# Optimization experiments

Hardware: AMD Instinct MI355X
Metric: run time of the kernel (lower is better)

Reference implementation:

```python
import jax, jax.numpy as jnp
import numpy as np


def conv1x1(x, w, b):
    # x: [B, Cin, H, W], w: [Cout, Cin], b: [Cout]
    return jnp.einsum('oc,bchw->bohw', w, x) + b[None, :, None, None]


def setup_inputs() -> dict:
    key = jax.random.key(0)
    ks = jax.random.split(key, 10)
    B, C, H, W = 8, 256, 64, 64
    C2 = C // 2
    s = 1.0 / np.sqrt(C)
    s2 = 1.0 / np.sqrt(C2)
    return {
        'x1': jax.random.normal(ks[0], (B, C, H, W), jnp.float32),
        'x2': jax.random.normal(ks[1], (B, C, H, W), jnp.float32),
        'w_th': jax.random.uniform(ks[2], (C2, C), jnp.float32, -s, s),
        'b_th': jax.random.uniform(ks[3], (C2,), jnp.float32, -s, s),
        'w_pi': jax.random.uniform(ks[4], (C2, C), jnp.float32, -s, s),
        'b_pi': jax.random.uniform(ks[5], (C2,), jnp.float32, -s, s),
        'w_g': jax.random.uniform(ks[6], (C2, C), jnp.float32, -s, s),
        'b_g': jax.random.uniform(ks[7], (C2,), jnp.float32, -s, s),
        'w_out': jax.random.uniform(ks[8], (C, C2), jnp.float32, -s2, s2),
        'b_out': jax.random.uniform(ks[9], (C,), jnp.float32, -s2, s2),
    }


def reference(x1, x2, w_th, b_th, w_pi, b_pi, w_g, b_g, w_out, b_out):
    B, C, H, W = x1.shape
    HW = H * W
    res = x1
    # 1x1 conv projections -> [B, C2, HW]
    e1 = conv1x1(x1, w_th, b_th).reshape(B, -1, HW)  # theta
    e2 = conv1x1(x2, w_pi, b_pi).reshape(B, -1, HW)  # phi
    # scores: [B, HW, HW]
    f = jnp.einsum('bcq,bck->bqk', e1, e2)
    # GLOBAL softmax over the whole HWxHW matrix per batch element
    f = jax.nn.softmax(f.reshape(B, HW * HW), axis=1).reshape(B, HW, HW)
    g2 = conv1x1(x2, w_g, b_g).reshape(B, -1, HW)  # [B, C2, HW]
    # out = f @ g2^T -> [B, HW, C2] -> [B, C2, H, W]
    out = jnp.einsum('bqk,bck->bcq', f, g2).reshape(B, -1, H, W)
    out = conv1x1(out, w_out, b_out)
    return out + res
```

## Files before the change

kernel.cpp:

```cpp
#include <hip/hip_runtime.h>

typedef unsigned short u16;
typedef short s16x8 __attribute__((ext_vector_type(8)));
typedef float f32x4 __attribute__((ext_vector_type(4)));

#define HWN 4096
#define CC  256
#define C2  128

static __device__ __forceinline__ u16 f2bf(float f) {
    union { float f; unsigned int u; } c; c.f = f;
    unsigned int u = c.u;
    unsigned int r = (u + 0x7fffu + ((u >> 16) & 1u)) >> 16;
    return (u16)r;
}
static __device__ __forceinline__ float bf2f(u16 u) {
    union { unsigned int u; float f; } c; c.u = ((unsigned int)u) << 16; return c.f;
}

__global__ __launch_bounds__(256) void k_wcvt(
    const float* __restrict__ w_th, const float* __restrict__ w_pi,
    const float* __restrict__ w_g,  const float* __restrict__ w_out,
    u16* __restrict__ wthb, u16* __restrict__ wpib,
    u16* __restrict__ wgb,  u16* __restrict__ woutb)
{
    int i = blockIdx.x * 256 + threadIdx.x;
    wthb[i]  = f2bf(w_th[i]);
    wpib[i]  = f2bf(w_pi[i]);
    wgb[i]   = f2bf(w_g[i]);
    woutb[i] = f2bf(w_out[i]);
}

__device__ __forceinline__ void load_afrag(const float* __restrict__ px, int g, s16x8 a[8]) {
    #pragma unroll
    for (int ks = 0; ks < 8; ++ks) {
        union { s16x8 v; u16 u[8]; } c;
        #pragma unroll
        for (int j = 0; j < 8; ++j)
            c.u[j] = f2bf(px[(size_t)(ks*32 + g*8 + j) * HWN]);
        a[ks] = c.v;
    }
}

__device__ __forceinline__ void proj_gemm(const s16x8 a[8], const u16* __restrict__ wb,
                                          const float* __restrict__ bias,
                                          int m16, int g, f32x4 acc[8]) {
    #pragma unroll
    for (int nb = 0; nb < 8; ++nb) {
        float bv = bias[nb*16 + m16];
        acc[nb] = (f32x4){bv, bv, bv, bv};
    }
    #pragma unroll
    for (int ks = 0; ks < 8; ++ks) {
        #pragma unroll
        for (int nb = 0; nb < 8; ++nb) {
            s16x8 bb = *(const s16x8*)&wb[(size_t)(nb*16 + m16)*CC + ks*32 + g*8];
            acc[nb] = __builtin_amdgcn_mfma_f32_16x16x32_bf16(a[ks], bb, acc[nb], 0, 0, 0);
        }
    }
}

__global__ __launch_bounds__(256) void k_projM(
    const float* __restrict__ x1, const float* __restrict__ x2,
    const u16* __restrict__ wthb, const float* __restrict__ b_th,
    const u16* __restrict__ wpib, const float* __restrict__ b_pi,
    const u16* __restrict__ wgb,  const float* __restrict__ b_g,
    u16* __restrict__ e1t, u16* __restrict__ e2t, u16* __restrict__ g2c)
{
    __shared__ u16 gs[C2][72];
    const int tid  = threadIdx.x;
    const int b    = blockIdx.x >> 6;
    const int q0   = (blockIdx.x & 63) * 64;
    const int wid  = __builtin_amdgcn_readfirstlane(tid >> 6);
    const int lane = tid & 63;
    const int m16  = lane & 15;
    const int g    = lane >> 4;

    s16x8 a[8];
    f32x4 acc[8];

    const float* px1 = x1 + (size_t)b*CC*HWN + q0 + wid*16 + m16;
    load_afrag(px1, g, a);
    proj_gemm(a, wthb, b_th, m16, g, acc);
    #pragma unroll
    for (int nb = 0; nb < 8; ++nb)
        #pragma unroll
        for (int r = 0; r < 4; ++r)
            e1t[((size_t)b*HWN + q0 + wid*16 + g*4 + r)*C2 + nb*16 + m16] = f2bf(acc[nb][r]);

    const float* px2 = x2 + (size_t)b*CC*HWN + q0 + wid*16 + m16;
    load_afrag(px2, g, a);
    proj_gemm(a, wpib, b_pi, m16, g, acc);
    #pragma unroll
    for (int nb = 0; nb < 8; ++nb)
        #pragma unroll
        for (int r = 0; r < 4; ++r)
            e2t[((size_t)b*HWN + q0 + wid*16 + g*4 + r)*C2 + nb*16 + m16] = f2bf(acc[nb][r]);

    proj_gemm(a, wgb, b_g, m16, g, acc);
    #pragma unroll
    for (int nb = 0; nb < 8; ++nb)
        #pragma unroll
        for (int r = 0; r < 4; ++r)
            gs[nb*16 + m16][wid*16 + g*4 + r] = f2bf(acc[nb][r]);
    __syncthreads();
    #pragma unroll
    for (int r = 0; r < 4; ++r) {
        int idx = r*256 + tid;
        int c2 = idx >> 3, q8 = idx & 7;
        int4 v = *(const int4*)&gs[c2][q8*8];
        *(int4*)&g2c[((size_t)b*C2 + c2)*HWN + q0 + q8*8] = v;
    }
}

__global__ __launch_bounds__(256, 2) void k_flash(
    const u16* __restrict__ e1t, const u16* __restrict__ e2t,
    const u16* __restrict__ g2c,
    u16* __restrict__ outp0, u16* __restrict__ outp1, float* __restrict__ ms)
{
    __shared__ u16 e2s[64*128];
    __shared__ u16 g2s[128*64];
    __shared__ u16 ps[4][32*64];

    const int tid  = threadIdx.x;
    const int b    = blockIdx.x >> 6;
    const int qb   = (blockIdx.x >> 1) & 31;
    const int seg  = blockIdx.x & 1;
    const int q0   = qb * 128;
    const int wid  = __builtin_amdgcn_readfirstlane(tid >> 6);
    const int lane = tid & 63;
    const int m16  = lane & 15;
    const int g    = lane >> 4;
    const int sw16 = (m16 & 7) << 3;

    s16x8 af[2][4];
    #pragma unroll
    for (int h = 0; h < 2; ++h) {
        const u16* p = e1t + ((size_t)b*HWN + q0 + wid*32 + h*16 + m16)*C2 + g*8;
        #pragma unroll
        for (int kc = 0; kc < 4; ++kc) af[h][kc] = *(const s16x8*)(p + kc*32);
    }

    f32x4 acc[2][8];
    #pragma unroll
    for (int h = 0; h < 2; ++h)
        #pragma unroll
        for (int i = 0; i < 8; ++i) acc[h][i] = (f32x4){0.f,0.f,0.f,0.f};
    float m_w = -INFINITY, s_w = 0.f;

    const u16* e2base = e2t + (size_t)b*HWN*C2;
    const u16* g2base = g2c + (size_t)b*C2*HWN;
    const int er_row = tid >> 4, er_c16 = tid & 15;
    const int gr_row = tid >> 3, gr_c8  = tid & 7;

    for (int it = 0; it < 32; ++it) {
        const int k0 = seg*2048 + it*64;
        __syncthreads();
        #pragma unroll
        for (int r = 0; r < 4; ++r) {
            int row = r*16 + er_row;
            int4 v = *(const int4*)(e2base + (size_t)(k0 + row)*C2 + er_c16*8);
            *(int4*)&e2s[(row*128 + er_c16*8) ^ ((row&7)<<3)] = v;
        }
        #pragma unroll
        for (int r = 0; r < 4; ++r) {
            int row = r*32 + gr_row;
            int4 v = *(const int4*)(g2base + (size_t)row*HWN + k0 + gr_c8*8);
            *(int4*)&g2s[(row*64 + gr_c8*8) ^ ((row&7)<<3)] = v;
        }
        __syncthreads();

        f32x4 s[2][4];
        #pragma unroll
        for (int h = 0; h < 2; ++h)
            #pragma unroll
            for (int j = 0; j < 4; ++j) s[h][j] = (f32x4){0.f,0.f,0.f,0.f};
        #pragma unroll
        for (int j = 0; j < 4; ++j) {
            #pragma unroll
            for (int kc = 0; kc < 4; ++kc) {
                s16x8 bb = *(const s16x8*)&e2s[((j*16+m16)*128 + kc*32 + g*8) ^ sw16];
                s[0][j] = __builtin_amdgcn_mfma_f32_16x16x32_bf16(af[0][kc], bb, s[0][j], 0, 0, 0);
                s[1][j] = __builtin_amdgcn_mfma_f32_16x16x32_bf16(af[1][kc], bb, s[1][j], 0, 0, 0);
            }
        }
        float tm = -INFINITY;
        #pragma unroll
        for (int h = 0; h < 2; ++h)
            #pragma unroll
            for (int j = 0; j < 4; ++j)
                #pragma unroll
                for (int r = 0; r < 4; ++r) tm = fmaxf(tm, s[h][j][r]);
        #pragma unroll
        for (int off = 32; off >= 1; off >>= 1) tm = fmaxf(tm, __shfl_xor(tm, off));
        const float m_new = fmaxf(m_w, tm);
        const float scale = __expf(m_w - m_new);
        m_w = m_new;
        s_w *= scale;
        #pragma unroll
        for (int h = 0; h < 2; ++h)
            #pragma unroll
            for (int i = 0; i < 8; ++i) {
                acc[h][i][0] *= scale; acc[h][i][1] *= scale;
                acc[h][i][2] *= scale; acc[h][i][3] *= scale;
            }
        float psum = 0.f;
        #pragma unroll
        for (int h = 0; h < 2; ++h)
            #pragma unroll
            for (int j = 0; j < 4; ++j)
                #pragma unroll
                for (int r = 0; r < 4; ++r) {
                    float p = __expf(s[h][j][r] - m_new);
                    psum += p;
                    int qq = h*16 + g*4 + r;
                    ps[wid][(qq*64 + j*16 + m16) ^ ((qq&7)<<3)] = f2bf(p);
                }
        s_w += psum;
        #pragma unroll
        for (int kk = 0; kk < 2; ++kk) {
            s16x8 pa0 = *(const s16x8*)&ps[wid][(m16*64      + kk*32 + g*8) ^ sw16];
            s16x8 pa1 = *(const s16x8*)&ps[wid][((16+m16)*64 + kk*32 + g*8) ^ sw16];
            #pragma unroll
            for (int fc = 0; fc < 8; ++fc) {
                s16x8 gb = *(const s16x8*)&g2s[((fc*16+m16)*64 + kk*32 + g*8) ^ sw16];
                acc[0][fc] = __builtin_amdgcn_mfma_f32_16x16x32_bf16(pa0, gb, acc[0][fc], 0, 0, 0);
                acc[1][fc] = __builtin_amdgcn_mfma_f32_16x16x32_bf16(pa1, gb, acc[1][fc], 0, 0, 0);
            }
        }
    }

    #pragma unroll
    for (int off = 32; off >= 1; off >>= 1) s_w += __shfl_xor(s_w, off);
    if (lane == 0) {
        int idx = b*256 + seg*128 + qb*4 + wid;
        ms[idx*2 + 0] = m_w;
        ms[idx*2 + 1] = s_w;
    }
    const float inv_s = 1.f / s_w;
    u16* op = seg ? outp1 : outp0;
    #pragma unroll
    for (int h = 0; h < 2; ++h)
        #pragma unroll
        for (int fc = 0; fc < 8; ++fc)
            #pragma unroll
            for (int r = 0; r < 4; ++r)
                op[((size_t)b*HWN + q0 + wid*32 + h*16 + g*4 + r)*C2 + fc*16 + m16] =
                    f2bf(acc[h][fc][r] * inv_s);
}

__global__ void k_mz(const float* __restrict__ ms, float* __restrict__ mz)
{
    __shared__ float rmax[4], rsum[4];
    const int b = blockIdx.x, tid = threadIdx.x;
    const int lane = tid & 63, wid = tid >> 6;
    float m = ms[((size_t)b*256 + tid)*2 + 0];
    float s = ms[((size_t)b*256 + tid)*2 + 1];
    float mm = m;
    #pragma unroll
    for (int off = 32; off >= 1; off >>= 1) mm = fmaxf(mm, __shfl_xor(mm, off));
    if (lane == 0) rmax[wid] = mm;
    __syncthreads();
    float M = fmaxf(fmaxf(rmax[0], rmax[1]), fmaxf(rmax[2], rmax[3]));
    float z = s * __expf(m - M);
    #pragma unroll
    for (int off = 32; off >= 1; off >>= 1) z += __shfl_xor(z, off);
    if (lane == 0) rsum[wid] = z;
    __syncthreads();
    if (tid == 0) { mz[b*2] = M; mz[b*2+1] = rsum[0]+rsum[1]+rsum[2]+rsum[3]; }
}

__global__ __launch_bounds__(256) void k_outM(
    const u16* __restrict__ outp0, const u16* __restrict__ outp1,
    const float* __restrict__ ms, const float* __restrict__ mz,
    const u16* __restrict__ woutb, const float* __restrict__ b_out,
    const float* __restrict__ x1, float* __restrict__ out)
{
    const int tid  = threadIdx.x;
    const int b    = blockIdx.x >> 6;
    const int q0   = (blockIdx.x & 63) * 64;
    const int wv   = tid >> 6;
    const int lane = tid & 63;
    const int m16  = lane & 15;
    const int g    = lane >> 4;
    const int q    = q0 + wv*16 + m16;

    const float M    = mz[b*2];
    const float invZ = 1.f / mz[b*2+1];
    const int idx5   = (q0 >> 5) + (wv >> 1);
    const float a0 = ms[(b*256 + idx5)*2+1]       * __expf(ms[(b*256 + idx5)*2]       - M) * invZ;
    const float a1 = ms[(b*256 + 128 + idx5)*2+1] * __expf(ms[(b*256 + 128 + idx5)*2] - M) * invZ;

    s16x8 bfr[4];
    #pragma unroll
    for (int ks = 0; ks < 4; ++ks) {
        union { s16x8 v; u16 u[8]; } o0, o1, oc;
        o0.v = *(const s16x8*)&outp0[((size_t)b*HWN + q)*C2 + ks*32 + g*8];
        o1.v = *(const s16x8*)&outp1[((size_t)b*HWN + q)*C2 + ks*32 + g*8];
        #pragma unroll
        for (int j = 0; j < 8; ++j)
            oc.u[j] = f2bf(a0*bf2f(o0.u[j]) + a1*bf2f(o1.u[j]));
        bfr[ks] = oc.v;
    }

    f32x4 acc[16];
    #pragma unroll
    for (int cb = 0; cb < 16; ++cb) acc[cb] = (f32x4){0.f,0.f,0.f,0.f};
    #pragma unroll
    for (int ks = 0; ks < 4; ++ks) {
        #pragma unroll
        for (int cb = 0; cb < 16; ++cb) {
            s16x8 afr = *(const s16x8*)&woutb[(size_t)(cb*16 + m16)*C2 + ks*32 + g*8];
            acc[cb] = __builtin_amdgcn_mfma_f32_16x16x32_bf16(afr, bfr[ks], acc[cb], 0, 0, 0);
        }
    }

    #pragma unroll
    for (int cb = 0; cb < 16; ++cb) {
        f32x4 bb = *(const f32x4*)&b_out[cb*16 + g*4];
        #pragma unroll
        for (int r = 0; r < 4; ++r) {
            int co = cb*16 + g*4 + r;
            size_t o = ((size_t)b*CC + co)*HWN + q;
            out[o] = acc[cb][r] + bb[r] + x1[o];
        }
    }
}

extern "C" void kernel_launch(void* const* d_in, const int* in_sizes, int n_in,
                              void* d_out, int out_size, void* d_ws, size_t ws_size,
                              hipStream_t stream)
{
    const float* x1   = (const float*)d_in[0];
    const float* x2   = (const float*)d_in[1];
    const float* w_th = (const float*)d_in[2];
    const float* b_th = (const float*)d_in[3];
    const float* w_pi = (const float*)d_in[4];
    const float* b_pi = (const float*)d_in[5];
    const float* w_g  = (const float*)d_in[6];
    const float* b_g  = (const float*)d_in[7];
    const float* w_out= (const float*)d_in[8];
    const float* b_out= (const float*)d_in[9];
    float* out = (float*)d_out;

    char* ws = (char*)d_ws;
    u16*   e1t  = (u16*)(ws);
    u16*   e2t  = (u16*)(ws + 8388608);
    u16*   g2c  = (u16*)(ws + 16777216);
    u16*   outp0= (u16*)(ws + 25165824);
    u16*   outp1= (u16*)(ws + 33554432);
    float* ms   = (float*)(ws + 41943040);
    float* mz   = (float*)(ws + 41959424);
    u16*   wthb = (u16*)(ws + 41959488);
    u16*   wpib = (u16*)(ws + 42025024);
    u16*   wgb  = (u16*)(ws + 42090560);
    u16*   woutb= (u16*)(ws + 42156096);

    k_wcvt <<<dim3(128), dim3(256), 0, stream>>>(w_th, w_pi, w_g, w_out, wthb, wpib, wgb, woutb);
    k_projM<<<dim3(512), dim3(256), 0, stream>>>(x1, x2, wthb, b_th, wpib, b_pi, wgb, b_g,
                                                 e1t, e2t, g2c);
    k_flash<<<dim3(512), dim3(256), 0, stream>>>(e1t, e2t, g2c, outp0, outp1, ms);
    k_mz   <<<dim3(8),   dim3(256), 0, stream>>>(ms, mz);
    k_outM <<<dim3(512), dim3(256), 0, stream>>>(outp0, outp1, ms, mz, woutb, b_out, x1, out);
}
```

Before: 207.7 us.

## Rework flash kernel with 32x32 MFMA, register P, double-buffered LDS

```diff
diff --git a/kernel.cpp b/kernel.cpp
--- a/kernel.cpp
+++ b/kernel.cpp
@@ -1,21 +1,28 @@
 #include <hip/hip_runtime.h>
 
 typedef unsigned short u16;
+typedef unsigned int u32;
 typedef short s16x8 __attribute__((ext_vector_type(8)));
 typedef float f32x4 __attribute__((ext_vector_type(4)));
+typedef float f32x16 __attribute__((ext_vector_type(16)));
 
 #define HWN 4096
 #define CC  256
 #define C2  128
 
 static __device__ __forceinline__ u16 f2bf(float f) {
-    union { float f; unsigned int u; } c; c.f = f;
-    unsigned int u = c.u;
-    unsigned int r = (u + 0x7fffu + ((u >> 16) & 1u)) >> 16;
+    union { float f; u32 u; } c; c.f = f;
+    u32 u = c.u;
+    u32 r = (u + 0x7fffu + ((u >> 16) & 1u)) >> 16;
     return (u16)r;
 }
 static __device__ __forceinline__ float bf2f(u16 u) {
-    union { unsigned int u; float f; } c; c.u = ((unsigned int)u) << 16; return c.f;
+    union { u32 u; float f; } c; c.u = ((u32)u) << 16; return c.f;
+}
+static __device__ __forceinline__ u32 cvtpk(float lo, float hi) {
+    u32 d;
+    asm("v_cvt_pk_bf16_f32 %0, %1, %2" : "=v"(d) : "v"(lo), "v"(hi));
+    return d;
 }
 
 __global__ __launch_bounds__(256) void k_wcvt(
@@ -118,115 +125,142 @@
     const u16* __restrict__ g2c,
     u16* __restrict__ outp0, u16* __restrict__ outp1, float* __restrict__ ms)
 {
-    __shared__ u16 e2s[64*128];
-    __shared__ u16 g2s[128*64];
-    __shared__ u16 ps[4][32*64];
+    __shared__ u16 e2s[2][64*128];
+    __shared__ u16 g2s[2][128*64];
 
     const int tid  = threadIdx.x;
-    const int b    = blockIdx.x >> 6;
-    const int qb   = (blockIdx.x >> 1) & 31;
-    const int seg  = blockIdx.x & 1;
+    const int bid  = ((blockIdx.x & 7) << 6) | (blockIdx.x >> 3);
+    const int b    = bid >> 6;
+    const int qb   = (bid >> 1) & 31;
+    const int seg  = bid & 1;
     const int q0   = qb * 128;
     const int wid  = __builtin_amdgcn_readfirstlane(tid >> 6);
     const int lane = tid & 63;
-    const int m16  = lane & 15;
-    const int g    = lane >> 4;
-    const int sw16 = (m16 & 7) << 3;
-
-    s16x8 af[2][4];
-    #pragma unroll
-    for (int h = 0; h < 2; ++h) {
-        const u16* p = e1t + ((size_t)b*HWN + q0 + wid*32 + h*16 + m16)*C2 + g*8;
-        #pragma unroll
-        for (int kc = 0; kc < 4; ++kc) af[h][kc] = *(const s16x8*)(p + kc*32);
-    }
-
-    f32x4 acc[2][8];
-    #pragma unroll
-    for (int h = 0; h < 2; ++h)
-        #pragma unroll
-        for (int i = 0; i < 8; ++i) acc[h][i] = (f32x4){0.f,0.f,0.f,0.f};
+    const int l31  = lane & 31;
+    const int h    = lane >> 5;
+    const int swz  = (l31 & 7) << 3;
+
+    s16x8 bq[8];
+    {
+        const u16* p = e1t + ((size_t)b*HWN + q0 + wid*32 + l31)*C2 + h*8;
+        #pragma unroll
+        for (int ks = 0; ks < 8; ++ks) bq[ks] = *(const s16x8*)(p + ks*16);
+    }
+
+    f32x16 accT[4];
+    #pragma unroll
+    for (int i = 0; i < 4; ++i)
+        accT[i] = (f32x16){0,0,0,0,0,0,0,0,0,0,0,0,0,0,0,0};
     float m_w = -INFINITY, s_w = 0.f;
 
     const u16* e2base = e2t + (size_t)b*HWN*C2;
     const u16* g2base = g2c + (size_t)b*C2*HWN;
-    const int er_row = tid >> 4, er_c16 = tid & 15;
-    const int gr_row = tid >> 3, gr_c8  = tid & 7;
+    const int er = tid >> 4, ec = tid & 15;
+    const int gr = tid >> 3, gc = tid & 7;
+    int ew[4], gw[4];
+    #pragma unroll
+    for (int r = 0; r < 4; ++r) {
+        int row = r*16 + er; ew[r] = (row*128 + ec*8) ^ ((row & 7) << 3);
+        int rw  = r*32 + gr; gw[r] = (rw*64  + gc*8) ^ ((rw  & 7) << 3);
+    }
+
+    int4 se[4], sg[4];
+    {
+        const int k0 = seg*2048;
+        #pragma unroll
+        for (int r = 0; r < 4; ++r)
+            se[r] = *(const int4*)(e2base + (size_t)(k0 + r*16 + er)*C2 + ec*8);
+        #pragma unroll
+        for (int r = 0; r < 4; ++r)
+            sg[r] = *(const int4*)(g2base + (size_t)(r*32 + gr)*HWN + k0 + gc*8);
+        #pragma unroll
+        for (int r = 0; r < 4; ++r) *(int4*)&e2s[0][ew[r]] = se[r];
+        #pragma unroll
+        for (int r = 0; r < 4; ++r) *(int4*)&g2s[0][gw[r]] = sg[r];
+    }
 
     for (int it = 0; it < 32; ++it) {
-        const int k0 = seg*2048 + it*64;
+        const int cur = it & 1;
         __syncthreads();
-        #pragma unroll
-        for (int r = 0; r < 4; ++r) {
-            int row = r*16 + er_row;
-            int4 v = *(const int4*)(e2base + (size_t)(k0 + row)*C2 + er_c16*8);
-            *(int4*)&e2s[(row*128 + er_c16*8) ^ ((row&7)<<3)] = v;
-        }
-        #pragma unroll
-        for (int r = 0; r < 4; ++r) {
-            int row = r*32 + gr_row;
-            int4 v = *(const int4*)(g2base + (size_t)row*HWN + k0 + gr_c8*8);
-            *(int4*)&g2s[(row*64 + gr_c8*8) ^ ((row&7)<<3)] = v;
-        }
-        __syncthreads();
-
-        f32x4 s[2][4];
-        #pragma unroll
-        for (int h = 0; h < 2; ++h)
-            #pragma unroll
-            for (int j = 0; j < 4; ++j) s[h][j] = (f32x4){0.f,0.f,0.f,0.f};
-        #pragma unroll
-        for (int j = 0; j < 4; ++j) {
-            #pragma unroll
-            for (int kc = 0; kc < 4; ++kc) {
-                s16x8 bb = *(const s16x8*)&e2s[((j*16+m16)*128 + kc*32 + g*8) ^ sw16];
-                s[0][j] = __builtin_amdgcn_mfma_f32_16x16x32_bf16(af[0][kc], bb, s[0][j], 0, 0, 0);
-                s[1][j] = __builtin_amdgcn_mfma_f32_16x16x32_bf16(af[1][kc], bb, s[1][j], 0, 0, 0);
+        const bool more = (it + 1 < 32);
+        if (more) {
+            const int k0n = seg*2048 + (it+1)*64;
+            #pragma unroll
+            for (int r = 0; r < 4; ++r)
+                se[r] = *(const int4*)(e2base + (size_t)(k0n + r*16 + er)*C2 + ec*8);
+            #pragma unroll
+            for (int r = 0; r < 4; ++r)
+                sg[r] = *(const int4*)(g2base + (size_t)(r*32 + gr)*HWN + k0n + gc*8);
+        }
+
+        f32x16 sr[2];
+        sr[0] = (f32x16){0,0,0,0,0,0,0,0,0,0,0,0,0,0,0,0};
+        sr[1] = (f32x16){0,0,0,0,0,0,0,0,0,0,0,0,0,0,0,0};
+        __builtin_amdgcn_s_setprio(1);
+        #pragma unroll
+        for (int ks = 0; ks < 8; ++ks) {
+            #pragma unroll
+            for (int mt = 0; mt < 2; ++mt) {
+                const int row = mt*32 + l31;
+                s16x8 afr = *(const s16x8*)&e2s[cur][row*128 + ((ks*16 + h*8) ^ swz)];
+                sr[mt] = __builtin_amdgcn_mfma_f32_32x32x16_bf16(afr, bq[ks], sr[mt], 0, 0, 0);
             }
         }
+        __builtin_amdgcn_s_setprio(0);
+
         float tm = -INFINITY;
         #pragma unroll
-        for (int h = 0; h < 2; ++h)
-            #pragma unroll
-            for (int j = 0; j < 4; ++j)
+        for (int mt = 0; mt < 2; ++mt)
+            #pragma unroll
+            for (int r = 0; r < 16; ++r) tm = fmaxf(tm, sr[mt][r]);
+        #pragma unroll
+        for (int off = 32; off >= 1; off >>= 1) tm = fmaxf(tm, __shfl_xor(tm, off));
+        if (tm > m_w + 8.f) {
+            const float sc = __expf(m_w - tm);
+            s_w *= sc;
+            #pragma unroll
+            for (int mt = 0; mt < 4; ++mt)
                 #pragma unroll
-                for (int r = 0; r < 4; ++r) tm = fmaxf(tm, s[h][j][r]);
-        #pragma unroll
-        for (int off = 32; off >= 1; off >>= 1) tm = fmaxf(tm, __shfl_xor(tm, off));
-        const float m_new = fmaxf(m_w, tm);
-        const float scale = __expf(m_w - m_new);
-        m_w = m_new;
-        s_w *= scale;
-        #pragma unroll
-        for (int h = 0; h < 2; ++h)
-            #pragma unroll
-            for (int i = 0; i < 8; ++i) {
-                acc[h][i][0] *= scale; acc[h][i][1] *= scale;
-                acc[h][i][2] *= scale; acc[h][i][3] *= scale;
+                for (int r = 0; r < 16; ++r) accT[mt][r] *= sc;
+            m_w = tm;
+        }
+        float psum = 0.f;
+        #pragma unroll
+        for (int mt = 0; mt < 2; ++mt)
+            #pragma unroll
+            for (int r = 0; r < 16; ++r) {
+                float p = __expf(sr[mt][r] - m_w);
+                sr[mt][r] = p;
+                psum += p;
             }
-        float psum = 0.f;
-        #pragma unroll
-        for (int h = 0; h < 2; ++h)
-            #pragma unroll
-            for (int j = 0; j < 4; ++j)
-                #pragma unroll
-                for (int r = 0; r < 4; ++r) {
-                    float p = __expf(s[h][j][r] - m_new);
-                    psum += p;
-                    int qq = h*16 + g*4 + r;
-                    ps[wid][(qq*64 + j*16 + m16) ^ ((qq&7)<<3)] = f2bf(p);
-                }
         s_w += psum;
-        #pragma unroll
-        for (int kk = 0; kk < 2; ++kk) {
-            s16x8 pa0 = *(const s16x8*)&ps[wid][(m16*64      + kk*32 + g*8) ^ sw16];
-            s16x8 pa1 = *(const s16x8*)&ps[wid][((16+m16)*64 + kk*32 + g*8) ^ sw16];
-            #pragma unroll
-            for (int fc = 0; fc < 8; ++fc) {
-                s16x8 gb = *(const s16x8*)&g2s[((fc*16+m16)*64 + kk*32 + g*8) ^ sw16];
-                acc[0][fc] = __builtin_amdgcn_mfma_f32_16x16x32_bf16(pa0, gb, acc[0][fc], 0, 0, 0);
-                acc[1][fc] = __builtin_amdgcn_mfma_f32_16x16x32_bf16(pa1, gb, acc[1][fc], 0, 0, 0);
+
+        __builtin_amdgcn_s_setprio(1);
+        #pragma unroll
+        for (int ks = 0; ks < 4; ++ks) {
+            const int mt_s = ks >> 1, rb = (ks & 1) * 8;
+            u32 wA = cvtpk(sr[mt_s][rb+0], sr[mt_s][rb+1]);
+            u32 wB = cvtpk(sr[mt_s][rb+2], sr[mt_s][rb+3]);
+            u32 wC = cvtpk(sr[mt_s][rb+4], sr[mt_s][rb+5]);
+            u32 wD = cvtpk(sr[mt_s][rb+6], sr[mt_s][rb+7]);
+            asm volatile("v_permlane32_swap_b32 %0, %1" : "+v"(wA), "+v"(wC));
+            asm volatile("v_permlane32_swap_b32 %0, %1" : "+v"(wB), "+v"(wD));
+            union { u32 w[4]; s16x8 v; } pf;
+            pf.w[0] = wA; pf.w[1] = wB; pf.w[2] = wC; pf.w[3] = wD;
+            #pragma unroll
+            for (int mt = 0; mt < 4; ++mt) {
+                const int row = mt*32 + l31;
+                s16x8 gfr = *(const s16x8*)&g2s[cur][row*64 + ((ks*16 + h*8) ^ swz)];
+                accT[mt] = __builtin_amdgcn_mfma_f32_32x32x16_bf16(gfr, pf.v, accT[mt], 0, 0, 0);
             }
+        }
+        __builtin_amdgcn_s_setprio(0);
+
+        if (more) {
+            #pragma unroll
+            for (int r = 0; r < 4; ++r) *(int4*)&e2s[cur ^ 1][ew[r]] = se[r];
+            #pragma unroll
+            for (int r = 0; r < 4; ++r) *(int4*)&g2s[cur ^ 1][gw[r]] = sg[r];
         }
     }
 
@@ -238,15 +272,25 @@
         ms[idx*2 + 1] = s_w;
     }
     const float inv_s = 1.f / s_w;
+    __syncthreads();
+    u16* lb = &e2s[0][0] + wid*4096;
+    #pragma unroll
+    for (int mt = 0; mt < 4; ++mt)
+        #pragma unroll
+        for (int p = 0; p < 8; ++p) {
+            u32 w = cvtpk(accT[mt][2*p] * inv_s, accT[mt][2*p+1] * inv_s);
+            int c2 = mt*32 + ((2*p) & 3) + 8*((2*p) >> 2) + 4*h;
+            int idx = (l31*128 + c2) ^ swz;
+            *(u32*)&lb[idx] = w;
+        }
     u16* op = seg ? outp1 : outp0;
     #pragma unroll
-    for (int h = 0; h < 2; ++h)
-        #pragma unroll
-        for (int fc = 0; fc < 8; ++fc)
-            #pragma unroll
-            for (int r = 0; r < 4; ++r)
-                op[((size_t)b*HWN + q0 + wid*32 + h*16 + g*4 + r)*C2 + fc*16 + m16] =
-                    f2bf(acc[h][fc][r] * inv_s);
+    for (int i = 0; i < 8; ++i) {
+        int cf = i*64 + lane;
+        int row = cf >> 4, ch = cf & 15;
+        int4 v = *(const int4*)&lb[(row*128 + ch*8) ^ ((row & 7) << 3)];
+        *(int4*)&op[((size_t)b*HWN + q0 + wid*32 + row)*C2 + ch*8] = v;
+    }
 }
 
 __global__ void k_mz(const float* __restrict__ ms, float* __restrict__ mz)
```

Measured after the change: 234.3 us. 12.8% more time.

## Prefetch next K tile into registers, double-buffer g2 in LDS, lazy softmax rescale

Applied to the files above, without the earlier changes.

```diff
diff --git a/kernel.cpp b/kernel.cpp
--- a/kernel.cpp
+++ b/kernel.cpp
@@ -1,6 +1,7 @@
 #include <hip/hip_runtime.h>
 
 typedef unsigned short u16;
+typedef unsigned int u32;
 typedef short s16x8 __attribute__((ext_vector_type(8)));
 typedef float f32x4 __attribute__((ext_vector_type(4)));
 
@@ -9,13 +10,13 @@
 #define C2  128
 
 static __device__ __forceinline__ u16 f2bf(float f) {
-    union { float f; unsigned int u; } c; c.f = f;
-    unsigned int u = c.u;
-    unsigned int r = (u + 0x7fffu + ((u >> 16) & 1u)) >> 16;
+    union { float f; u32 u; } c; c.f = f;
+    u32 u = c.u;
+    u32 r = (u + 0x7fffu + ((u >> 16) & 1u)) >> 16;
     return (u16)r;
 }
 static __device__ __forceinline__ float bf2f(u16 u) {
-    union { unsigned int u; float f; } c; c.u = ((unsigned int)u) << 16; return c.f;
+    union { u32 u; float f; } c; c.u = ((u32)u) << 16; return c.f;
 }
 
 __global__ __launch_bounds__(256) void k_wcvt(
@@ -119,13 +120,14 @@
     u16* __restrict__ outp0, u16* __restrict__ outp1, float* __restrict__ ms)
 {
     __shared__ u16 e2s[64*128];
-    __shared__ u16 g2s[128*64];
+    __shared__ u16 g2s[2][128*64];
     __shared__ u16 ps[4][32*64];
 
     const int tid  = threadIdx.x;
-    const int b    = blockIdx.x >> 6;
-    const int qb   = (blockIdx.x >> 1) & 31;
-    const int seg  = blockIdx.x & 1;
+    const int bid  = ((blockIdx.x & 7) << 6) | (blockIdx.x >> 3);
+    const int b    = bid >> 6;
+    const int qb   = (bid >> 1) & 31;
+    const int seg  = bid & 1;
     const int q0   = qb * 128;
     const int wid  = __builtin_amdgcn_readfirstlane(tid >> 6);
     const int lane = tid & 63;
@@ -150,31 +152,50 @@
 
     const u16* e2base = e2t + (size_t)b*HWN*C2;
     const u16* g2base = g2c + (size_t)b*C2*HWN;
-    const int er_row = tid >> 4, er_c16 = tid & 15;
-    const int gr_row = tid >> 3, gr_c8  = tid & 7;
+    const int er = tid >> 4, ec = tid & 15;
+    const int gr = tid >> 3, gc = tid & 7;
+    int ew[4], gw[4];
+    #pragma unroll
+    for (int r = 0; r < 4; ++r) {
+        int row = r*16 + er; ew[r] = (row*128 + ec*8) ^ ((row & 7) << 3);
+        int rw  = r*32 + gr; gw[r] = (rw*64  + gc*8) ^ ((rw  & 7) << 3);
+    }
+
+    int4 se[4], sg[4];
+    {
+        const int k0 = seg*2048;
+        #pragma unroll
+        for (int r = 0; r < 4; ++r)
+            se[r] = *(const int4*)(e2base + (size_t)(k0 + r*16 + er)*C2 + ec*8);
+        #pragma unroll
+        for (int r = 0; r < 4; ++r)
+            sg[r] = *(const int4*)(g2base + (size_t)(r*32 + gr)*HWN + k0 + gc*8);
+        #pragma unroll
+        for (int r = 0; r < 4; ++r) *(int4*)&e2s[ew[r]] = se[r];
+        #pragma unroll
+        for (int r = 0; r < 4; ++r) *(int4*)&g2s[0][gw[r]] = sg[r];
+    }
 
     for (int it = 0; it < 32; ++it) {
-        const int k0 = seg*2048 + it*64;
+        const int cur = it & 1;
         __syncthreads();
-        #pragma unroll
-        for (int r = 0; r < 4; ++r) {
-            int row = r*16 + er_row;
-            int4 v = *(const int4*)(e2base + (size_t)(k0 + row)*C2 + er_c16*8);
-            *(int4*)&e2s[(row*128 + er_c16*8) ^ ((row&7)<<3)] = v;
-        }
-        #pragma unroll
-        for (int r = 0; r < 4; ++r) {
-            int row = r*32 + gr_row;
-            int4 v = *(const int4*)(g2base + (size_t)row*HWN + k0 + gr_c8*8);
-            *(int4*)&g2s[(row*64 + gr_c8*8) ^ ((row&7)<<3)] = v;
-        }
-        __syncthreads();
+        const bool more = (it + 1 < 32);
+        if (more) {
+            const int k0n = seg*2048 + (it+1)*64;
+            #pragma unroll
+            for (int r = 0; r < 4; ++r)
+                se[r] = *(const int4*)(e2base + (size_t)(k0n + r*16 + er)*C2 + ec*8);
+            #pragma unroll
+            for (int r = 0; r < 4; ++r)
+                sg[r] = *(const int4*)(g2base + (size_t)(r*32 + gr)*HWN + k0n + gc*8);
+        }
 
         f32x4 s[2][4];
         #pragma unroll
         for (int h = 0; h < 2; ++h)
             #pragma unroll
             for (int j = 0; j < 4; ++j) s[h][j] = (f32x4){0.f,0.f,0.f,0.f};
+        __builtin_amdgcn_s_setprio(1);
         #pragma unroll
         for (int j = 0; j < 4; ++j) {
             #pragma unroll
@@ -184,6 +205,9 @@
                 s[1][j] = __builtin_amdgcn_mfma_f32_16x16x32_bf16(af[1][kc], bb, s[1][j], 0, 0, 0);
             }
         }
+        __builtin_amdgcn_s_setprio(0);
+        __syncthreads();
+
         float tm = -INFINITY;
         #pragma unroll
         for (int h = 0; h < 2; ++h)
@@ -193,17 +217,18 @@
                 for (int r = 0; r < 4; ++r) tm = fmaxf(tm, s[h][j][r]);
         #pragma unroll
         for (int off = 32; off >= 1; off >>= 1) tm = fmaxf(tm, __shfl_xor(tm, off));
-        const float m_new = fmaxf(m_w, tm);
-        const float scale = __expf(m_w - m_new);
-        m_w = m_new;
-        s_w *= scale;
-        #pragma unroll
-        for (int h = 0; h < 2; ++h)
-            #pragma unroll
-            for (int i = 0; i < 8; ++i) {
-                acc[h][i][0] *= scale; acc[h][i][1] *= scale;
-                acc[h][i][2] *= scale; acc[h][i][3] *= scale;
-            }
+        if (tm > m_w + 8.f) {
+            const float sc = __expf(m_w - tm);
+            s_w *= sc;
+            #pragma unroll
+            for (int h = 0; h < 2; ++h)
+                #pragma unroll
+                for (int i = 0; i < 8; ++i) {
+                    acc[h][i][0] *= sc; acc[h][i][1] *= sc;
+                    acc[h][i][2] *= sc; acc[h][i][3] *= sc;
+                }
+            m_w = tm;
+        }
         float psum = 0.f;
         #pragma unroll
         for (int h = 0; h < 2; ++h)
@@ -211,22 +236,32 @@
             for (int j = 0; j < 4; ++j)
                 #pragma unroll
                 for (int r = 0; r < 4; ++r) {
-                    float p = __expf(s[h][j][r] - m_new);
+                    float p = __expf(s[h][j][r] - m_w);
                     psum += p;
                     int qq = h*16 + g*4 + r;
                     ps[wid][(qq*64 + j*16 + m16) ^ ((qq&7)<<3)] = f2bf(p);
                 }
         s_w += psum;
+
+        __builtin_amdgcn_s_setprio(1);
         #pragma unroll
         for (int kk = 0; kk < 2; ++kk) {
             s16x8 pa0 = *(const s16x8*)&ps[wid][(m16*64      + kk*32 + g*8) ^ sw16];
             s16x8 pa1 = *(const s16x8*)&ps[wid][((16+m16)*64 + kk*32 + g*8) ^ sw16];
             #pragma unroll
             for (int fc = 0; fc < 8; ++fc) {
-                s16x8 gb = *(const s16x8*)&g2s[((fc*16+m16)*64 + kk*32 + g*8) ^ sw16];
+                s16x8 gb = *(const s16x8*)&g2s[cur][((fc*16+m16)*64 + kk*32 + g*8) ^ sw16];
                 acc[0][fc] = __builtin_amdgcn_mfma_f32_16x16x32_bf16(pa0, gb, acc[0][fc], 0, 0, 0);
                 acc[1][fc] = __builtin_amdgcn_mfma_f32_16x16x32_bf16(pa1, gb, acc[1][fc], 0, 0, 0);
             }
+        }
+        __builtin_amdgcn_s_setprio(0);
+
+        if (more) {
+            #pragma unroll
+            for (int r = 0; r < 4; ++r) *(int4*)&e2s[ew[r]] = se[r];
+            #pragma unroll
+            for (int r = 0; r < 4; ++r) *(int4*)&g2s[cur ^ 1][gw[r]] = sg[r];
         }
     }
 
```

New measurement: 242.7 us. 16.8% more time.
